# Kernel tuning notes

Measured on AMD Instinct MI355X. Metric: run time of the kernel, lower is better.

## Reference

```python
import jax, jax.numpy as jnp
import numpy as np
from jax import lax

ALPHA = 0.98
DELTA = 2.0
R = 0.5
S = 0.025
EPS = 1e-6


def setup_inputs() -> dict:
    key = jax.random.key(0)
    # non-negative energy spectrogram [B, n_mels, T]
    x = jax.random.uniform(key, (64, 128, 4000), dtype=jnp.float32)
    return {"x": x}


def _pcen(x):
    # x: [B, C, T]; EMA smoother: smooth[0] = x[0], smooth[t] = (1-s)*smooth[t-1] + s*x[t]
    xt = jnp.moveaxis(x, -1, 0)  # [T, B, C]

    def step(carry, x_t):
        sm = (1.0 - S) * carry + S * x_t
        return sm, sm

    init = xt[0]
    _, sm_rest = lax.scan(step, init, xt[1:])  # [T-1, B, C]
    smooth = jnp.concatenate([init[None], sm_rest], axis=0)  # [T, B, C]
    smooth = jnp.moveaxis(smooth, 0, -1)  # [B, C, T]
    pcen = (x / (smooth + EPS) ** ALPHA + DELTA) ** R - DELTA ** R
    return pcen


def reference(x):
    return _pcen(x)
```

## Files before the change

### kernel.cpp

```cpp
#include <hip/hip_runtime.h>
#include <math.h>


constexpr int   TLEN = 4000;
constexpr int   NF4  = 1000;
constexpr int   NTH  = 256;
constexpr int   KPL  = 16;
constexpr float S_C  = 0.025f;
constexpr float A_1  = 1.0f - S_C;

constexpr float fpow(float b, int n) {
    float r = 1.0f;
    for (int i = 0; i < n; ++i) r *= b;
    return r;
}
constexpr float A_2  = fpow(A_1, 2);
constexpr float A_3  = fpow(A_1, 3);
constexpr float A256 = fpow(A_1, 256);

constexpr float L2A4 = -0.14610359f;

constexpr float ALPHA = 0.98f;
constexpr float EPS_C = 1e-6f;
constexpr float SQRT2 = 1.41421356237309515f;

__device__ __forceinline__ float pcen_elem(float x, float sm) {
    float t = sm + EPS_C;
    float p = __builtin_amdgcn_exp2f(-ALPHA * __builtin_amdgcn_logf(t));
    float y = fmaf(x, p, 2.0f);
    return __builtin_amdgcn_sqrtf(y) - SQRT2;
}

__global__ __launch_bounds__(NTH) void pcen_kernel(const float* __restrict__ x,
                                                   float* __restrict__ out,
                                                   int nch) {
    const int lane = threadIdx.x & 63;
    const int ch   = blockIdx.x * (NTH / 64) + (threadIdx.x >> 6);
    if (ch >= nch) return;

    const size_t base = (size_t)ch * TLEN;
    const float4* __restrict__ x4 = (const float4*)(x + base);
    float4*       __restrict__ o4 = (float4*)(out + base);

    float4 v[KPL];
#pragma unroll
    for (int k = 0; k < KPL; ++k) {
        int f4 = lane + 64 * k;
        v[k] = (f4 < NF4) ? x4[f4] : make_float4(0.f, 0.f, 0.f, 0.f);
    }

    float B[KPL];
#pragma unroll
    for (int k = 0; k < KPL; ++k) {
        float4 r  = v[k];
        float  b0 = (lane == 0 && k == 0) ? r.x : S_C * r.x;
        B[k] = fmaf(A_3, b0, S_C * fmaf(A_2, r.y, fmaf(A_1, r.z, r.w)));
    }

    constexpr float CD[6] = { fpow(A_1, 4),  fpow(A_1, 8),  fpow(A_1, 16),
                              fpow(A_1, 32), fpow(A_1, 64), fpow(A_1, 128) };
#pragma unroll
    for (int s = 0; s < 6; ++s) {
        const int   d  = 1 << s;
        const float cc = CD[s];
        float Bp[KPL];
#pragma unroll
        for (int k = 0; k < KPL; ++k) Bp[k] = __shfl_up(B[k], d);
        const bool ok = (lane >= d);
#pragma unroll
        for (int k = 0; k < KPL; ++k)
            B[k] = fmaf(cc, ok ? Bp[k] : 0.0f, B[k]);
    }

    const float Al = __builtin_amdgcn_exp2f((float)lane * L2A4);

    float e = 0.0f;
#pragma unroll
    for (int k = 0; k < KPL; ++k) {
        float Tk = (k < KPL - 1) ? __shfl(B[k], 63) : 0.0f;
        float Bi = __shfl_up(B[k], 1);
        if (lane == 0) Bi = 0.0f;
        float sm = fmaf(Al, e, Bi);

        float4 r  = v[k];
        float  b0 = (lane == 0 && k == 0) ? r.x : S_C * r.x;
        float  s0 = fmaf(A_1, sm, b0);
        float  s1 = fmaf(A_1, s0, S_C * r.y);
        float  s2 = fmaf(A_1, s1, S_C * r.z);
        float  s3 = fmaf(A_1, s2, S_C * r.w);

        float4 o;
        o.x = pcen_elem(r.x, s0);
        o.y = pcen_elem(r.y, s1);
        o.z = pcen_elem(r.z, s2);
        o.w = pcen_elem(r.w, s3);

        int f4 = lane + 64 * k;
        if (f4 < NF4) o4[f4] = o;

        e = fmaf(A256, e, Tk);
    }
}

extern "C" void kernel_launch(void* const* d_in, const int* in_sizes, int n_in,
                              void* d_out, int out_size, void* d_ws, size_t ws_size,
                              hipStream_t stream) {
    const float* x   = (const float*)d_in[0];
    float*       out = (float*)d_out;
    const int nch    = in_sizes[0] / TLEN;
    const int wpb    = NTH / 64;
    const int grid   = (nch + wpb - 1) / wpb;
    pcen_kernel<<<grid, NTH, 0, stream>>>(x, out, nch);
}
```

Baseline: 228.3 us.

## Software-pipeline per-wave scan in groups with two-group load prefetch

```diff
diff --git a/kernel.cpp b/kernel.cpp
--- a/kernel.cpp
+++ b/kernel.cpp
@@ -6,6 +6,8 @@
 constexpr int   NF4  = 1000;
 constexpr int   NTH  = 256;
 constexpr int   KPL  = 16;
+constexpr int   G    = 4;
+constexpr int   NG   = KPL / G;
 constexpr float S_C  = 0.025f;
 constexpr float A_1  = 1.0f - S_C;
 
@@ -43,62 +45,81 @@
     float4*       __restrict__ o4 = (float4*)(out + base);
 
     float4 v[KPL];
+    float  B[KPL];
+
 #pragma unroll
-    for (int k = 0; k < KPL; ++k) {
+    for (int k = 0; k < 2 * G; ++k) {
         int f4 = lane + 64 * k;
         v[k] = (f4 < NF4) ? x4[f4] : make_float4(0.f, 0.f, 0.f, 0.f);
     }
 
-    float B[KPL];
-#pragma unroll
-    for (int k = 0; k < KPL; ++k) {
-        float4 r  = v[k];
-        float  b0 = (lane == 0 && k == 0) ? r.x : S_C * r.x;
-        B[k] = fmaf(A_3, b0, S_C * fmaf(A_2, r.y, fmaf(A_1, r.z, r.w)));
-    }
-
     constexpr float CD[6] = { fpow(A_1, 4),  fpow(A_1, 8),  fpow(A_1, 16),
                               fpow(A_1, 32), fpow(A_1, 64), fpow(A_1, 128) };
-#pragma unroll
-    for (int s = 0; s < 6; ++s) {
-        const int   d  = 1 << s;
-        const float cc = CD[s];
-        float Bp[KPL];
-#pragma unroll
-        for (int k = 0; k < KPL; ++k) Bp[k] = __shfl_up(B[k], d);
-        const bool ok = (lane >= d);
-#pragma unroll
-        for (int k = 0; k < KPL; ++k)
-            B[k] = fmaf(cc, ok ? Bp[k] : 0.0f, B[k]);
-    }
 
     const float Al = __builtin_amdgcn_exp2f((float)lane * L2A4);
 
     float e = 0.0f;
+
 #pragma unroll
-    for (int k = 0; k < KPL; ++k) {
-        float Tk = (k < KPL - 1) ? __shfl(B[k], 63) : 0.0f;
-        float Bi = __shfl_up(B[k], 1);
-        if (lane == 0) Bi = 0.0f;
-        float sm = fmaf(Al, e, Bi);
+    for (int g = 0; g < NG; ++g) {
+        if (g + 2 < NG) {
+#pragma unroll
+            for (int j = 0; j < G; ++j) {
+                int k  = (g + 2) * G + j;
+                int f4 = lane + 64 * k;
+                v[k] = (f4 < NF4) ? x4[f4] : make_float4(0.f, 0.f, 0.f, 0.f);
+            }
+        }
 
-        float4 r  = v[k];
-        float  b0 = (lane == 0 && k == 0) ? r.x : S_C * r.x;
-        float  s0 = fmaf(A_1, sm, b0);
-        float  s1 = fmaf(A_1, s0, S_C * r.y);
-        float  s2 = fmaf(A_1, s1, S_C * r.z);
-        float  s3 = fmaf(A_1, s2, S_C * r.w);
+#pragma unroll
+        for (int j = 0; j < G; ++j) {
+            const int k = g * G + j;
+            float4 r  = v[k];
+            float  b0 = (lane == 0 && k == 0) ? r.x : S_C * r.x;
+            B[k] = fmaf(A_3, b0, S_C * fmaf(A_2, r.y, fmaf(A_1, r.z, r.w)));
+        }
 
-        float4 o;
-        o.x = pcen_elem(r.x, s0);
-        o.y = pcen_elem(r.y, s1);
-        o.z = pcen_elem(r.z, s2);
-        o.w = pcen_elem(r.w, s3);
+#pragma unroll
+        for (int s = 0; s < 6; ++s) {
+            const int   d  = 1 << s;
+            const float cc = CD[s];
+            float Bp[G];
+#pragma unroll
+            for (int j = 0; j < G; ++j) Bp[j] = __shfl_up(B[g * G + j], d);
+            const bool ok = (lane >= d);
+#pragma unroll
+            for (int j = 0; j < G; ++j) {
+                const int k = g * G + j;
+                B[k] = fmaf(cc, ok ? Bp[j] : 0.0f, B[k]);
+            }
+        }
 
-        int f4 = lane + 64 * k;
-        if (f4 < NF4) o4[f4] = o;
+#pragma unroll
+        for (int j = 0; j < G; ++j) {
+            const int k  = g * G + j;
+            float Tk = (k < KPL - 1) ? __shfl(B[k], 63) : 0.0f;
+            float Bi = __shfl_up(B[k], 1);
+            if (lane == 0) Bi = 0.0f;
+            float sm = fmaf(Al, e, Bi);
 
-        e = fmaf(A256, e, Tk);
+            float4 r  = v[k];
+            float  b0 = (lane == 0 && k == 0) ? r.x : S_C * r.x;
+            float  s0 = fmaf(A_1, sm, b0);
+            float  s1 = fmaf(A_1, s0, S_C * r.y);
+            float  s2 = fmaf(A_1, s1, S_C * r.z);
+            float  s3 = fmaf(A_1, s2, S_C * r.w);
+
+            float4 o;
+            o.x = pcen_elem(r.x, s0);
+            o.y = pcen_elem(r.y, s1);
+            o.z = pcen_elem(r.z, s2);
+            o.w = pcen_elem(r.w, s3);
+
+            int f4 = lane + 64 * k;
+            if (f4 < NF4) o4[f4] = o;
+
+            e = fmaf(A256, e, Tk);
+        }
     }
 }
 
```

New measurement: 229.2 us. About the same (+0.4%).

## Process two channels per wave with software-pipelined half-channel loads

Applied to the files above, without the earlier changes.

```diff
diff --git a/kernel.cpp b/kernel.cpp
--- a/kernel.cpp
+++ b/kernel.cpp
@@ -5,9 +5,11 @@
 constexpr int   TLEN = 4000;
 constexpr int   NF4  = 1000;
 constexpr int   NTH  = 256;
-constexpr int   KPL  = 16;
+constexpr int   HALF = 8;
 constexpr float S_C  = 0.025f;
 constexpr float A_1  = 1.0f - S_C;
+
+typedef float f4_t __attribute__((ext_vector_type(4)));
 
 constexpr float fpow(float b, int n) {
     float r = 1.0f;
@@ -31,75 +33,104 @@
     return __builtin_amdgcn_sqrtf(y) - SQRT2;
 }
 
-__global__ __launch_bounds__(NTH) void pcen_kernel(const float* __restrict__ x,
-                                                   float* __restrict__ out,
-                                                   int nch) {
-    const int lane = threadIdx.x & 63;
-    const int ch   = blockIdx.x * (NTH / 64) + (threadIdx.x >> 6);
-    if (ch >= nch) return;
+__device__ __forceinline__ void load_half(f4_t (&v)[HALF], const f4_t* __restrict__ x4,
+                                          int lane, int h ) {
+#pragma unroll
+    for (int j = 0; j < HALF; ++j) {
+        const int f4 = lane + 64 * (h * HALF + j);
+        v[j] = (f4 < NF4) ? x4[f4] : (f4_t){0.f, 0.f, 0.f, 0.f};
+    }
+}
 
-    const size_t base = (size_t)ch * TLEN;
-    const float4* __restrict__ x4 = (const float4*)(x + base);
-    float4*       __restrict__ o4 = (float4*)(out + base);
-
-    float4 v[KPL];
-#pragma unroll
-    for (int k = 0; k < KPL; ++k) {
-        int f4 = lane + 64 * k;
-        v[k] = (f4 < NF4) ? x4[f4] : make_float4(0.f, 0.f, 0.f, 0.f);
-    }
-
-    float B[KPL];
-#pragma unroll
-    for (int k = 0; k < KPL; ++k) {
-        float4 r  = v[k];
-        float  b0 = (lane == 0 && k == 0) ? r.x : S_C * r.x;
-        B[k] = fmaf(A_3, b0, S_C * fmaf(A_2, r.y, fmaf(A_1, r.z, r.w)));
-    }
-
+__device__ __forceinline__ void compute_half(const f4_t (&v)[HALF], f4_t* __restrict__ o4,
+                                             int lane, float Al, float& e,
+                                             int h, bool store_ok) {
     constexpr float CD[6] = { fpow(A_1, 4),  fpow(A_1, 8),  fpow(A_1, 16),
                               fpow(A_1, 32), fpow(A_1, 64), fpow(A_1, 128) };
+    float B[HALF];
+#pragma unroll
+    for (int j = 0; j < HALF; ++j) {
+        f4_t  r  = v[j];
+        float b0 = (h == 0 && j == 0 && lane == 0) ? r.x : S_C * r.x;
+        B[j] = fmaf(A_3, b0, S_C * fmaf(A_2, r.y, fmaf(A_1, r.z, r.w)));
+    }
 #pragma unroll
     for (int s = 0; s < 6; ++s) {
         const int   d  = 1 << s;
         const float cc = CD[s];
-        float Bp[KPL];
+        float Bp[HALF];
 #pragma unroll
-        for (int k = 0; k < KPL; ++k) Bp[k] = __shfl_up(B[k], d);
+        for (int j = 0; j < HALF; ++j) Bp[j] = __shfl_up(B[j], d);
         const bool ok = (lane >= d);
 #pragma unroll
-        for (int k = 0; k < KPL; ++k)
-            B[k] = fmaf(cc, ok ? Bp[k] : 0.0f, B[k]);
+        for (int j = 0; j < HALF; ++j) B[j] = fmaf(cc, ok ? Bp[j] : 0.0f, B[j]);
     }
-
-    const float Al = __builtin_amdgcn_exp2f((float)lane * L2A4);
-
-    float e = 0.0f;
 #pragma unroll
-    for (int k = 0; k < KPL; ++k) {
-        float Tk = (k < KPL - 1) ? __shfl(B[k], 63) : 0.0f;
-        float Bi = __shfl_up(B[k], 1);
+    for (int j = 0; j < HALF; ++j) {
+        const int k  = h * HALF + j;
+        float Tk = __shfl(B[j], 63);
+        float Bi = __shfl_up(B[j], 1);
         if (lane == 0) Bi = 0.0f;
         float sm = fmaf(Al, e, Bi);
 
-        float4 r  = v[k];
-        float  b0 = (lane == 0 && k == 0) ? r.x : S_C * r.x;
-        float  s0 = fmaf(A_1, sm, b0);
-        float  s1 = fmaf(A_1, s0, S_C * r.y);
-        float  s2 = fmaf(A_1, s1, S_C * r.z);
-        float  s3 = fmaf(A_1, s2, S_C * r.w);
+        f4_t  r  = v[j];
+        float b0 = (h == 0 && j == 0 && lane == 0) ? r.x : S_C * r.x;
+        float s0 = fmaf(A_1, sm, b0);
+        float s1 = fmaf(A_1, s0, S_C * r.y);
+        float s2 = fmaf(A_1, s1, S_C * r.z);
+        float s3 = fmaf(A_1, s2, S_C * r.w);
 
-        float4 o;
+        f4_t o;
         o.x = pcen_elem(r.x, s0);
         o.y = pcen_elem(r.y, s1);
         o.z = pcen_elem(r.z, s2);
         o.w = pcen_elem(r.w, s3);
 
-        int f4 = lane + 64 * k;
-        if (f4 < NF4) o4[f4] = o;
+        const int f4 = lane + 64 * k;
+        if (store_ok && f4 < NF4) __builtin_nontemporal_store(o, &o4[f4]);
 
         e = fmaf(A256, e, Tk);
     }
+}
+
+__global__ __launch_bounds__(NTH) void pcen_kernel(const float* __restrict__ x,
+                                                   float* __restrict__ out,
+                                                   int nch) {
+    const int lane = threadIdx.x & 63;
+    const int wid  = blockIdx.x * (NTH / 64) + (threadIdx.x >> 6);
+    const int nw   = gridDim.x * (NTH / 64);
+    const int c0   = wid;
+    const int c1   = wid + nw;
+    if (c0 >= nch) return;
+    const bool has1 = (c1 < nch);
+
+    const f4_t* __restrict__ x0 = (const f4_t*)(x + (size_t)c0 * TLEN);
+    const f4_t* __restrict__ x1 = (const f4_t*)(x + (size_t)(has1 ? c1 : c0) * TLEN);
+    f4_t*       __restrict__ o0 = (f4_t*)(out + (size_t)c0 * TLEN);
+    f4_t*       __restrict__ o1 = (f4_t*)(out + (size_t)(has1 ? c1 : c0) * TLEN);
+
+    const float Al = __builtin_amdgcn_exp2f((float)lane * L2A4);
+
+    f4_t  va[HALF], vb[HALF];
+    float e = 0.0f;
+
+    load_half(va, x0, lane, 0);
+    __builtin_amdgcn_sched_barrier(0);
+
+    load_half(vb, x0, lane, 1);
+    __builtin_amdgcn_sched_barrier(0);
+    compute_half(va, o0, lane, Al, e, 0, true);
+
+    load_half(va, x1, lane, 0);
+    __builtin_amdgcn_sched_barrier(0);
+    compute_half(vb, o0, lane, Al, e, 1, true);
+
+    e = 0.0f;
+    load_half(vb, x1, lane, 1);
+    __builtin_amdgcn_sched_barrier(0);
+    compute_half(va, o1, lane, Al, e, 0, has1);
+
+    compute_half(vb, o1, lane, Al, e, 1, has1);
 }
 
 extern "C" void kernel_launch(void* const* d_in, const int* in_sizes, int n_in,
@@ -109,6 +140,7 @@
     float*       out = (float*)d_out;
     const int nch    = in_sizes[0] / TLEN;
     const int wpb    = NTH / 64;
-    const int grid   = (nch + wpb - 1) / wpb;
+    const int nw     = (nch + 1) / 2;
+    const int grid   = (nw + wpb - 1) / wpb;
     pcen_kernel<<<grid, NTH, 0, stream>>>(x, out, nch);
 }
```

Result: no change. 231.8 us (+1.5%).
